# Kernel tuning notes

Hardware: AMD Instinct MI355X
Metric: run time of the kernel (lower is better)

The kernel has to match this reference:

```python
import jax, jax.numpy as jnp
import numpy as np

B = 65536
N_SPARSE = 26
N_DENSE = 13
EMB = 5
VOCAB = 100000
N_EXPERTS = 4
D_IN = N_DENSE + N_SPARSE * EMB  # 143
H1, H2 = 128, 64


def setup_inputs() -> dict:
    key = jax.random.key(0)
    ks = jax.random.split(key, 16)
    s = 0.05
    return {
        "sparse_inputs": jax.random.randint(ks[0], (B, N_SPARSE), 0, VOCAB),
        "dense_inputs": jax.random.normal(ks[1], (B, N_DENSE), dtype=jnp.float32),
        "emb_tables": jax.random.normal(ks[2], (N_SPARSE, VOCAB, EMB), dtype=jnp.float32) * s,
        "expert_W1": jax.random.normal(ks[3], (N_EXPERTS, D_IN, H1), dtype=jnp.float32) * s,
        "expert_b1": jnp.zeros((N_EXPERTS, H1), dtype=jnp.float32),
        "expert_W2": jax.random.normal(ks[4], (N_EXPERTS, H1, H2), dtype=jnp.float32) * s,
        "expert_b2": jnp.zeros((N_EXPERTS, H2), dtype=jnp.float32),
        "gate_finish_W": jax.random.normal(ks[5], (D_IN, N_EXPERTS), dtype=jnp.float32) * s,
        "gate_finish_b": jnp.zeros((N_EXPERTS,), dtype=jnp.float32),
        "gate_like_W": jax.random.normal(ks[6], (D_IN, N_EXPERTS), dtype=jnp.float32) * s,
        "gate_like_b": jnp.zeros((N_EXPERTS,), dtype=jnp.float32),
        "finish_W": jax.random.normal(ks[7], (H2, 1), dtype=jnp.float32) * s,
        "finish_b": jnp.zeros((1,), dtype=jnp.float32),
        "like_W": jax.random.normal(ks[8], (H2, 1), dtype=jnp.float32) * s,
        "like_b": jnp.zeros((1,), dtype=jnp.float32),
    }


def reference(sparse_inputs, dense_inputs, emb_tables, expert_W1, expert_b1,
              expert_W2, expert_b2, gate_finish_W, gate_finish_b,
              gate_like_W, gate_like_b, finish_W, finish_b, like_W, like_b):
    # per-feature embedding lookup: [B, N_SPARSE, EMB]
    feat_idx = jnp.arange(N_SPARSE)[None, :]
    sp_emb = emb_tables[feat_idx, sparse_inputs]
    x = jnp.concatenate([dense_inputs, sp_emb.reshape(sparse_inputs.shape[0], -1)], axis=1)  # [B, D_IN]

    # batched expert MLPs (dropout is inactive at inference)
    h = jax.nn.relu(jnp.einsum('bd,edh->beh', x, expert_W1) + expert_b1)  # [B, E, 128]
    expert_out = jax.nn.relu(jnp.einsum('beh,eho->beo', h, expert_W2) + expert_b2)  # [B, E, 64]

    gate_f = jax.nn.softmax(x @ gate_finish_W + gate_finish_b, axis=-1)  # [B, E]
    gate_l = jax.nn.softmax(x @ gate_like_W + gate_like_b, axis=-1)

    task_finish = jnp.einsum('be,beo->bo', gate_f, expert_out)  # [B, 64]
    task_like = jnp.einsum('be,beo->bo', gate_l, expert_out)

    finish = jax.nn.sigmoid(task_finish @ finish_W + finish_b)  # [B, 1]
    like = jax.nn.sigmoid(task_like @ like_W + like_b)  # [B, 1]
    return finish, like
```

## Files before the change

### kernel.cpp

```cpp
#include <hip/hip_runtime.h>
#include <math.h>

#define NB     65536
#define NSP    26
#define NDN    13
#define EMBD   5
#define VOCAB  100000
#define NE     4
#define DIN    143
#define KPAD   160
#define H1     128
#define H2     64

typedef __attribute__((ext_vector_type(8))) short bf16x8;
typedef __attribute__((ext_vector_type(4))) float f32x4;

__device__ __forceinline__ unsigned short f2bf(float f) {
    unsigned int u = __float_as_uint(f);
    u = (u + 0x7fff + ((u >> 16) & 1)) >> 16;
    return (unsigned short)u;
}

#define E1 (4*8*5*512)
#define E2 (4*4*4*512)
#define E3 (5*512)
#define NWE (E1+E2+E3)
#define GBLKS 1024
#define PBLKS ((NWE+255)/256)


__global__ __launch_bounds__(256)
void gather_pack(const int*   __restrict__ sparse,
                 const float* __restrict__ dense,
                 const float* __restrict__ emb,
                 const float* __restrict__ W1,  const float* __restrict__ W2,
                 const float* __restrict__ gfW, const float* __restrict__ glW,
                 unsigned short* __restrict__ w1p, unsigned short* __restrict__ w2p,
                 unsigned short* __restrict__ gwp, unsigned short* __restrict__ xg)
{
    const int blk = blockIdx.x;
    const int tid = threadIdx.x;
    if (blk < GBLKS) {
        __shared__ int idxs[64 * NSP];
        __shared__ __align__(16) unsigned short xs[64][168];
        const int row0 = blk * 64;

        for (int t = tid; t < 64 * NSP; t += 256)
            idxs[t] = sparse[row0 * NSP + t];
        for (int t = tid; t < 64 * NDN; t += 256) {
            int r = t / NDN, c = t - r * NDN;
            xs[r][c] = f2bf(dense[(row0 + r) * NDN + c]);
        }
        for (int t = tid; t < 64 * (KPAD - DIN); t += 256) {
            int r = t / (KPAD - DIN), c = DIN + (t - r * (KPAD - DIN));
            xs[r][c] = 0;
        }
        __syncthreads();
        for (int t = tid; t < 64 * NSP * EMBD; t += 256) {
            int f = t / (64 * EMBD);
            int rem = t - f * (64 * EMBD);
            int r = rem / EMBD, c = rem - r * EMBD;
            int idx = idxs[r * NSP + f];
            float v = emb[((size_t)f * VOCAB + idx) * EMBD + c];
            xs[r][NDN + f * EMBD + c] = f2bf(v);
        }
        __syncthreads();
        for (int v = tid; v < 4 * 5 * 64; v += 256) {
            int lo = v & 63, chunk = v >> 6;
            int s = chunk % 5, tl = chunk / 5;
            int b = lo & 15, g = lo >> 4;
            bf16x8 val = *(const bf16x8*)&xs[tl * 16 + b][32 * s + 8 * g];
            *(bf16x8*)(xg + ((size_t)((blk * 4 + tl) * 5 + s) * 64 + lo) * 8) = val;
        }
        return;
    }

    int i = (blk - GBLKS) * 256 + tid;
    if (i < E1) {
        int j = i & 7, l = (i >> 3) & 63;
        int rest = i >> 9;
        int s = rest % 5; rest /= 5;
        int nt = rest & 7, e = rest >> 3;
        int b = l & 15, g = l >> 4;
        int k = 32 * s + 8 * g + j;
        int n = nt * 16 + b;
        w1p[i] = (k < DIN) ? f2bf(W1[(e * DIN + k) * H1 + n]) : (unsigned short)0;
        return;
    }
    i -= E1;
    if (i < E2) {
        int j = i & 7, l = (i >> 3) & 63;
        int rest = i >> 9;
        int s = rest & 3; rest >>= 2;
        int ot = rest & 3, e = rest >> 2;
        int b = l & 15, g = l >> 4;
        int k = 32 * s + 8 * g + j;
        int o = ot * 16 + b;
        w2p[i] = f2bf(W2[(e * H1 + k) * H2 + o]);
        return;
    }
    i -= E2;
    if (i < E3) {
        int j = i & 7, l = (i >> 3) & 63;
        int s = i >> 9;
        int b = l & 15, g = l >> 4;
        int k = 32 * s + 8 * g + j;
        float v = 0.f;
        if (k < DIN) {
            if (b < 4)      v = gfW[k * NE + b];
            else if (b < 8) v = glW[k * NE + (b - 4)];
        }
        gwp[i] = f2bf(v);
    }
}

__global__ __launch_bounds__(512, 1)
void mmoe5(const unsigned short* __restrict__ xg,
           const unsigned short* __restrict__ w1p, const float* __restrict__ b1,
           const unsigned short* __restrict__ w2p, const float* __restrict__ b2,
           const unsigned short* __restrict__ gwp,
           const float* __restrict__ gfb, const float* __restrict__ glb,
           const float* __restrict__ fW,  const float* __restrict__ fb,
           const float* __restrict__ lW,  const float* __restrict__ lb,
           float* __restrict__ out)
{
    __shared__ __align__(16) unsigned short wlds[28672];
    __shared__ __align__(16) char hsb[16 * 4096];
    __shared__ float gts[256][8];

    const int tid  = threadIdx.x;
    const int wid  = tid >> 6;
    const int lane = tid & 63;
    const int b    = lane & 15;
    const int g    = lane >> 4;
    const int t0   = blockIdx.x * 16 + wid * 2;
    const int swz  = (b & 7) << 4;
    char* const hw = hsb + (wid * 2) * 4096 + b * 256;

    bf16x8 xf[2][5];
    #pragma unroll
    for (int rt = 0; rt < 2; ++rt)
        #pragma unroll
        for (int s = 0; s < 5; ++s)
            xf[rt][s] = *(const bf16x8*)(xg + ((size_t)((t0 + rt) * 5 + s) * 64 + lane) * 8);

    f32x4 ga[2];
    ga[0] = (f32x4){0.f, 0.f, 0.f, 0.f};
    ga[1] = (f32x4){0.f, 0.f, 0.f, 0.f};
    #pragma unroll
    for (int s = 0; s < 5; ++s) {
        bf16x8 af = *(const bf16x8*)(gwp + (size_t)(s * 64 + lane) * 8);
        ga[0] = __builtin_amdgcn_mfma_f32_16x16x32_bf16(af, xf[0][s], ga[0], 0, 0, 0);
        ga[1] = __builtin_amdgcn_mfma_f32_16x16x32_bf16(af, xf[1][s], ga[1], 0, 0, 0);
    }
    if (g < 2) {
        const float4 bias = *(const float4*)(g ? glb : gfb);
        #pragma unroll
        for (int rt = 0; rt < 2; ++rt) {
            float l0 = ga[rt][0] + bias.x, l1 = ga[rt][1] + bias.y;
            float l2 = ga[rt][2] + bias.z, l3 = ga[rt][3] + bias.w;
            float m = fmaxf(fmaxf(l0, l1), fmaxf(l2, l3));
            float e0 = expf(l0 - m), e1 = expf(l1 - m), e2 = expf(l2 - m), e3 = expf(l3 - m);
            float inv = 1.f / (e0 + e1 + e2 + e3);
            float4 gv; gv.x = e0 * inv; gv.y = e1 * inv; gv.z = e2 * inv; gv.w = e3 * inv;
            *(float4*)&gts[wid * 32 + rt * 16 + b][g * 4] = gv;
        }
    }

    float vf[2] = {0.f, 0.f}, vl[2] = {0.f, 0.f};
    for (int e = 0; e < NE; ++e) {
        __syncthreads();
        #pragma unroll
        for (int v = tid; v < 2560; v += 512)
            *(bf16x8*)(wlds + v * 8) = *(const bf16x8*)(w1p + (size_t)e * 20480 + v * 8);
        #pragma unroll
        for (int v = tid; v < 1024; v += 512)
            *(bf16x8*)(wlds + 20480 + v * 8) = *(const bf16x8*)(w2p + (size_t)e * 8192 + v * 8);
        __syncthreads();

        #pragma unroll
        for (int nt = 0; nt < 8; ++nt) {
            bf16x8 wv[5];
            #pragma unroll
            for (int s = 0; s < 5; ++s)
                wv[s] = *(const bf16x8*)(wlds + ((nt * 5 + s) * 64 + lane) * 8);
            f32x4 acc[2];
            acc[0] = (f32x4){0.f, 0.f, 0.f, 0.f};
            acc[1] = (f32x4){0.f, 0.f, 0.f, 0.f};
            #pragma unroll
            for (int s = 0; s < 5; ++s) {
                acc[0] = __builtin_amdgcn_mfma_f32_16x16x32_bf16(wv[s], xf[0][s], acc[0], 0, 0, 0);
                acc[1] = __builtin_amdgcn_mfma_f32_16x16x32_bf16(wv[s], xf[1][s], acc[1], 0, 0, 0);
            }
            const float4 b1v = *(const float4*)(b1 + e * H1 + nt * 16 + 4 * g);
            #pragma unroll
            for (int rt = 0; rt < 2; ++rt) {
                unsigned lo = (unsigned)f2bf(fmaxf(acc[rt][0] + b1v.x, 0.f)) |
                              ((unsigned)f2bf(fmaxf(acc[rt][1] + b1v.y, 0.f)) << 16);
                unsigned hi = (unsigned)f2bf(fmaxf(acc[rt][2] + b1v.z, 0.f)) |
                              ((unsigned)f2bf(fmaxf(acc[rt][3] + b1v.w, 0.f)) << 16);
                uint2 hv; hv.x = lo; hv.y = hi;
                *(uint2*)(hw + rt * 4096 + ((nt * 32 + g * 8) ^ swz)) = hv;
            }
        }

        bf16x8 hf[2][4];
        #pragma unroll
        for (int rt = 0; rt < 2; ++rt)
            #pragma unroll
            for (int s = 0; s < 4; ++s)
                hf[rt][s] = *(const bf16x8*)(hw + rt * 4096 + ((s * 64 + g * 16) ^ swz));

        float gfv[2], glv[2];
        #pragma unroll
        for (int rt = 0; rt < 2; ++rt) {
            gfv[rt] = gts[wid * 32 + rt * 16 + b][e];
            glv[rt] = gts[wid * 32 + rt * 16 + b][4 + e];
        }

        #pragma unroll
        for (int ot = 0; ot < 4; ++ot) {
            bf16x8 wv2[4];
            #pragma unroll
            for (int s = 0; s < 4; ++s)
                wv2[s] = *(const bf16x8*)(wlds + 20480 + ((ot * 4 + s) * 64 + lane) * 8);
            f32x4 c[2];
            c[0] = (f32x4){0.f, 0.f, 0.f, 0.f};
            c[1] = (f32x4){0.f, 0.f, 0.f, 0.f};
            #pragma unroll
            for (int s = 0; s < 4; ++s) {
                c[0] = __builtin_amdgcn_mfma_f32_16x16x32_bf16(wv2[s], hf[0][s], c[0], 0, 0, 0);
                c[1] = __builtin_amdgcn_mfma_f32_16x16x32_bf16(wv2[s], hf[1][s], c[1], 0, 0, 0);
            }
            const float4 b2v = *(const float4*)(b2 + e * H2 + ot * 16 + 4 * g);
            const float4 fwv = *(const float4*)(fW + ot * 16 + 4 * g);
            const float4 lwv = *(const float4*)(lW + ot * 16 + 4 * g);
            #pragma unroll
            for (int rt = 0; rt < 2; ++rt) {
                float o0 = fmaxf(c[rt][0] + b2v.x, 0.f), o1 = fmaxf(c[rt][1] + b2v.y, 0.f);
                float o2 = fmaxf(c[rt][2] + b2v.z, 0.f), o3 = fmaxf(c[rt][3] + b2v.w, 0.f);
                vf[rt] += gfv[rt] * (o0 * fwv.x + o1 * fwv.y + o2 * fwv.z + o3 * fwv.w);
                vl[rt] += glv[rt] * (o0 * lwv.x + o1 * lwv.y + o2 * lwv.z + o3 * lwv.w);
            }
        }
    }

    #pragma unroll
    for (int rt = 0; rt < 2; ++rt) {
        float f = vf[rt], l = vl[rt];
        f += __shfl_xor(f, 16); f += __shfl_xor(f, 32);
        l += __shfl_xor(l, 16); l += __shfl_xor(l, 32);
        if (g == 0) {
            int r = (t0 + rt) * 16 + b;
            out[r]      = 1.f / (1.f + expf(-(f + fb[0])));
            out[NB + r] = 1.f / (1.f + expf(-(l + lb[0])));
        }
    }
}


__global__ __launch_bounds__(256)
void preproc(const float* __restrict__ W1, const float* __restrict__ W2,
             const float* __restrict__ gfW, const float* __restrict__ glW,
             unsigned short* __restrict__ w1t, unsigned short* __restrict__ w2t,
             unsigned short* __restrict__ gwc)
{
    int i = blockIdx.x * 256 + threadIdx.x;
    if (i < 4*128*160) {
        int k = i % KPAD;
        int n = (i / KPAD) & (H1 - 1);
        int e = i / (KPAD * H1);
        w1t[i] = (k < DIN) ? f2bf(W1[(e * DIN + k) * H1 + n]) : (unsigned short)0;
    } else if (i < 4*128*160 + 4*64*128) {
        int j = i - 4*128*160;
        int k = j & (H1 - 1);
        int o = (j >> 7) & (H2 - 1);
        int e = j >> 13;
        w2t[j] = f2bf(W2[(e * H1 + k) * H2 + o]);
    } else if (i < 4*128*160 + 4*64*128 + 16*160) {
        int j = i - (4*128*160 + 4*64*128);
        int k = j % KPAD;
        int r = j / KPAD;
        float v = 0.f;
        if (k < DIN) {
            if (r < 4)      v = gfW[k * NE + r];
            else if (r < 8) v = glW[k * NE + (r - 4)];
        }
        gwc[j] = f2bf(v);
    }
}

__global__ __launch_bounds__(256)
void mmoe_mfma(const int*   __restrict__ sparse,
               const float* __restrict__ dense,
               const float* __restrict__ emb,
               const unsigned short* __restrict__ w1t,
               const float* __restrict__ b1,
               const unsigned short* __restrict__ w2t,
               const float* __restrict__ b2,
               const unsigned short* __restrict__ gwc,
               const float* __restrict__ gfb, const float* __restrict__ glb,
               const float* __restrict__ fW,  const float* __restrict__ fb,
               const float* __restrict__ lW,  const float* __restrict__ lb,
               float* __restrict__ out)
{
    __shared__ __align__(16) unsigned short xs[64][KPAD];
    __shared__ __align__(16) unsigned short hs[64][136];
    __shared__ __align__(16) float gts[64][8];

    const int tid   = threadIdx.x;
    const int wid   = tid >> 6;
    const int lane  = tid & 63;
    const int b     = lane & 15;
    const int g     = lane >> 4;
    const int rbase = wid * 16;
    const int grow0 = blockIdx.x * 64 + rbase;

    for (int t = lane; t < 16 * NDN; t += 64) {
        int r = t & 15, d = t >> 4;
        xs[rbase + r][d] = f2bf(dense[(grow0 + r) * NDN + d]);
    }
    for (int t = lane; t < 16 * (KPAD - DIN); t += 64) {
        int r = t & 15, d = DIN + (t >> 4);
        xs[rbase + r][d] = 0;
    }
    for (int t = lane; t < 16 * NSP; t += 64) {
        int r = t & 15, f = t >> 4;
        int idx = sparse[(grow0 + r) * NSP + f];
        const float* ep = emb + (f * VOCAB + idx) * EMBD;
        int c0 = NDN + EMBD * f;
        #pragma unroll
        for (int c = 0; c < EMBD; ++c)
            xs[rbase + r][c0 + c] = f2bf(ep[c]);
    }

    bf16x8 xf[5];
    #pragma unroll
    for (int s = 0; s < 5; ++s)
        xf[s] = *(const bf16x8*)&xs[rbase + b][32 * s + 8 * g];

    f32x4 ga = {0.f, 0.f, 0.f, 0.f};
    #pragma unroll
    for (int s = 0; s < 5; ++s) {
        bf16x8 af = *(const bf16x8*)(gwc + b * KPAD + 32 * s + 8 * g);
        ga = __builtin_amdgcn_mfma_f32_16x16x32_bf16(af, xf[s], ga, 0, 0, 0);
    }
    if (g < 2) {
        const float4 bias = *(const float4*)(g ? glb : gfb);
        float l0 = ga[0] + bias.x, l1 = ga[1] + bias.y;
        float l2 = ga[2] + bias.z, l3 = ga[3] + bias.w;
        float m = fmaxf(fmaxf(l0, l1), fmaxf(l2, l3));
        float e0 = expf(l0 - m), e1 = expf(l1 - m), e2 = expf(l2 - m), e3 = expf(l3 - m);
        float inv = 1.f / (e0 + e1 + e2 + e3);
        float4 gv; gv.x = e0 * inv; gv.y = e1 * inv; gv.z = e2 * inv; gv.w = e3 * inv;
        *(float4*)&gts[rbase + b][g * 4] = gv;
    }

    float vf = 0.f, vl = 0.f;
    for (int e = 0; e < NE; ++e) {
        const unsigned short* w1e = w1t + e * (H1 * KPAD);
        #pragma unroll
        for (int nt = 0; nt < 8; ++nt) {
            f32x4 acc = {0.f, 0.f, 0.f, 0.f};
            #pragma unroll
            for (int s = 0; s < 5; ++s) {
                bf16x8 af = *(const bf16x8*)(w1e + (nt * 16 + b) * KPAD + 32 * s + 8 * g);
                acc = __builtin_amdgcn_mfma_f32_16x16x32_bf16(af, xf[s], acc, 0, 0, 0);
            }
            const float4 b1v = *(const float4*)(b1 + e * H1 + nt * 16 + 4 * g);
            unsigned lo = (unsigned)f2bf(fmaxf(acc[0] + b1v.x, 0.f)) |
                          ((unsigned)f2bf(fmaxf(acc[1] + b1v.y, 0.f)) << 16);
            unsigned hi = (unsigned)f2bf(fmaxf(acc[2] + b1v.z, 0.f)) |
                          ((unsigned)f2bf(fmaxf(acc[3] + b1v.w, 0.f)) << 16);
            uint2 hv; hv.x = lo; hv.y = hi;
            *(uint2*)&hs[rbase + b][nt * 16 + 4 * g] = hv;
        }

        bf16x8 hf[4];
        #pragma unroll
        for (int s = 0; s < 4; ++s)
            hf[s] = *(const bf16x8*)&hs[rbase + b][32 * s + 8 * g];

        float gf = gts[rbase + b][e];
        float gl = gts[rbase + b][4 + e];
        const unsigned short* w2e = w2t + e * (H2 * H1);
        #pragma unroll
        for (int ot = 0; ot < 4; ++ot) {
            f32x4 acc = {0.f, 0.f, 0.f, 0.f};
            #pragma unroll
            for (int s = 0; s < 4; ++s) {
                bf16x8 af = *(const bf16x8*)(w2e + (ot * 16 + b) * H1 + 32 * s + 8 * g);
                acc = __builtin_amdgcn_mfma_f32_16x16x32_bf16(af, hf[s], acc, 0, 0, 0);
            }
            const float4 b2v = *(const float4*)(b2 + e * H2 + ot * 16 + 4 * g);
            const float4 fwv = *(const float4*)(fW + ot * 16 + 4 * g);
            const float4 lwv = *(const float4*)(lW + ot * 16 + 4 * g);
            float o0 = fmaxf(acc[0] + b2v.x, 0.f);
            float o1 = fmaxf(acc[1] + b2v.y, 0.f);
            float o2 = fmaxf(acc[2] + b2v.z, 0.f);
            float o3 = fmaxf(acc[3] + b2v.w, 0.f);
            vf += gf * (o0 * fwv.x + o1 * fwv.y + o2 * fwv.z + o3 * fwv.w);
            vl += gl * (o0 * lwv.x + o1 * lwv.y + o2 * lwv.z + o3 * lwv.w);
        }
    }

    vf += __shfl_xor(vf, 16); vf += __shfl_xor(vf, 32);
    vl += __shfl_xor(vl, 16); vl += __shfl_xor(vl, 32);
    if (g == 0) {
        int r = grow0 + b;
        out[r]      = 1.f / (1.f + expf(-(vf + fb[0])));
        out[NB + r] = 1.f / (1.f + expf(-(vl + lb[0])));
    }
}


extern "C" void kernel_launch(void* const* d_in, const int* in_sizes, int n_in,
                              void* d_out, int out_size, void* d_ws, size_t ws_size,
                              hipStream_t stream) {
    const int*   sparse = (const int*)  d_in[0];
    const float* dense  = (const float*)d_in[1];
    const float* emb    = (const float*)d_in[2];
    const float* W1     = (const float*)d_in[3];
    const float* b1     = (const float*)d_in[4];
    const float* W2     = (const float*)d_in[5];
    const float* b2     = (const float*)d_in[6];
    const float* gfW    = (const float*)d_in[7];
    const float* gfb    = (const float*)d_in[8];
    const float* glW    = (const float*)d_in[9];
    const float* glb    = (const float*)d_in[10];
    const float* fW     = (const float*)d_in[11];
    const float* fb     = (const float*)d_in[12];
    const float* lW     = (const float*)d_in[13];
    const float* lb     = (const float*)d_in[14];

    const size_t XG_BYTES = (size_t)NB * KPAD * 2;
    const size_t NEED = XG_BYTES + (size_t)NWE * 2;

    if (ws_size >= NEED) {
        unsigned short* xg  = (unsigned short*)d_ws;
        unsigned short* w1p = (unsigned short*)((char*)d_ws + XG_BYTES);
        unsigned short* w2p = (unsigned short*)((char*)d_ws + XG_BYTES + (size_t)E1 * 2);
        unsigned short* gwp = (unsigned short*)((char*)d_ws + XG_BYTES + (size_t)(E1 + E2) * 2);

        gather_pack<<<GBLKS + PBLKS, 256, 0, stream>>>(
            sparse, dense, emb, W1, W2, gfW, glW, w1p, w2p, gwp, xg);
        mmoe5<<<NB / 256, 512, 0, stream>>>(xg, w1p, b1, w2p, b2, gwp,
                                            gfb, glb, fW, fb, lW, lb,
                                            (float*)d_out);
    } else {
        unsigned short* w1t = (unsigned short*)d_ws;
        unsigned short* w2t = (unsigned short*)((char*)d_ws + 163840);
        unsigned short* gwc = (unsigned short*)((char*)d_ws + 229376);

        int tot = 4*128*160 + 4*64*128 + 16*160;
        preproc<<<(tot + 255) / 256, 256, 0, stream>>>(W1, W2, gfW, glW, w1t, w2t, gwc);
        mmoe_mfma<<<NB / 64, 256, 0, stream>>>(sparse, dense, emb,
                                               w1t, b1, w2t, b2, gwc,
                                               gfb, glb, fW, fb, lW, lb,
                                               (float*)d_out);
    }
}
```

Before: 62.97 us.

## Prefetch next expert weights into registers, split layer-2 into halves, smaller blocks

The MMoE kernel now runs 256-thread blocks with two blocks per CU (was one 512-thread block), each covering 128 rows. The next expert's weights are prefetched into registers while the current expert computes, so global loads overlap with the MFMA work. The hidden layer is split into two halves with layer-2 accumulation done per half, which halves the LDS staging buffer for activations. Bf16 packing now uses the hardware v_cvt_pk_bf16_f32 instruction instead of software rounding. In exchange, register pressure rises from the prefetch buffers and layer-2 accumulators, and each weight tile is loaded by twice as many blocks.

```diff
diff --git a/kernel.cpp b/kernel.cpp
--- a/kernel.cpp
+++ b/kernel.cpp
@@ -19,6 +19,12 @@
     unsigned int u = __float_as_uint(f);
     u = (u + 0x7fff + ((u >> 16) & 1)) >> 16;
     return (unsigned short)u;
+}
+
+__device__ __forceinline__ unsigned cvtpk(float lo, float hi) {
+    unsigned r;
+    asm("v_cvt_pk_bf16_f32 %0, %1, %2" : "=v"(r) : "v"(lo), "v"(hi));
+    return r;
 }
 
 #define E1 (4*8*5*512)
@@ -114,8 +120,8 @@
     }
 }
 
-__global__ __launch_bounds__(512, 1)
-void mmoe5(const unsigned short* __restrict__ xg,
+__global__ __launch_bounds__(256, 2)
+void mmoe7(const unsigned short* __restrict__ xg,
            const unsigned short* __restrict__ w1p, const float* __restrict__ b1,
            const unsigned short* __restrict__ w2p, const float* __restrict__ b2,
            const unsigned short* __restrict__ gwp,
@@ -124,18 +130,18 @@
            const float* __restrict__ lW,  const float* __restrict__ lb,
            float* __restrict__ out)
 {
-    __shared__ __align__(16) unsigned short wlds[28672];
-    __shared__ __align__(16) char hsb[16 * 4096];
-    __shared__ float gts[256][8];
+    __shared__ __align__(16) char wlds[57344];
+    __shared__ __align__(16) char hsb[16384];
+    __shared__ float gts[128][8];
 
     const int tid  = threadIdx.x;
     const int wid  = tid >> 6;
     const int lane = tid & 63;
     const int b    = lane & 15;
     const int g    = lane >> 4;
-    const int t0   = blockIdx.x * 16 + wid * 2;
+    const int t0   = blockIdx.x * 8 + wid * 2;
     const int swz  = (b & 7) << 4;
-    char* const hw = hsb + (wid * 2) * 4096 + b * 256;
+    char* const hw = hsb + wid * 4096 + b * 128;
 
     bf16x8 xf[2][5];
     #pragma unroll
@@ -143,6 +149,14 @@
         #pragma unroll
         for (int s = 0; s < 5; ++s)
             xf[rt][s] = *(const bf16x8*)(xg + ((size_t)((t0 + rt) * 5 + s) * 64 + lane) * 8);
+
+    bf16x8 pw1[10], pw2[4];
+    #pragma unroll
+    for (int i = 0; i < 10; ++i)
+        pw1[i] = *(const bf16x8*)(w1p + (size_t)(tid + i * 256) * 8);
+    #pragma unroll
+    for (int i = 0; i < 4; ++i)
+        pw2[i] = *(const bf16x8*)(w2p + (size_t)(tid + i * 256) * 8);
 
     f32x4 ga[2];
     ga[0] = (f32x4){0.f, 0.f, 0.f, 0.f};
@@ -171,45 +185,70 @@
     for (int e = 0; e < NE; ++e) {
         __syncthreads();
         #pragma unroll
-        for (int v = tid; v < 2560; v += 512)
-            *(bf16x8*)(wlds + v * 8) = *(const bf16x8*)(w1p + (size_t)e * 20480 + v * 8);
-        #pragma unroll
-        for (int v = tid; v < 1024; v += 512)
-            *(bf16x8*)(wlds + 20480 + v * 8) = *(const bf16x8*)(w2p + (size_t)e * 8192 + v * 8);
+        for (int i = 0; i < 10; ++i)
+            *(bf16x8*)(wlds + (tid + i * 256) * 16) = pw1[i];
+        #pragma unroll
+        for (int i = 0; i < 4; ++i)
+            *(bf16x8*)(wlds + 40960 + (tid + i * 256) * 16) = pw2[i];
+        if (e < 3) {
+            #pragma unroll
+            for (int i = 0; i < 10; ++i)
+                pw1[i] = *(const bf16x8*)(w1p + (size_t)(e + 1) * 20480 + (size_t)(tid + i * 256) * 8);
+            #pragma unroll
+            for (int i = 0; i < 4; ++i)
+                pw2[i] = *(const bf16x8*)(w2p + (size_t)(e + 1) * 8192 + (size_t)(tid + i * 256) * 8);
+        }
         __syncthreads();
 
-        #pragma unroll
-        for (int nt = 0; nt < 8; ++nt) {
-            bf16x8 wv[5];
-            #pragma unroll
-            for (int s = 0; s < 5; ++s)
-                wv[s] = *(const bf16x8*)(wlds + ((nt * 5 + s) * 64 + lane) * 8);
-            f32x4 acc[2];
-            acc[0] = (f32x4){0.f, 0.f, 0.f, 0.f};
-            acc[1] = (f32x4){0.f, 0.f, 0.f, 0.f};
-            #pragma unroll
-            for (int s = 0; s < 5; ++s) {
-                acc[0] = __builtin_amdgcn_mfma_f32_16x16x32_bf16(wv[s], xf[0][s], acc[0], 0, 0, 0);
-                acc[1] = __builtin_amdgcn_mfma_f32_16x16x32_bf16(wv[s], xf[1][s], acc[1], 0, 0, 0);
+        f32x4 c[2][4];
+        #pragma unroll
+        for (int rt = 0; rt < 2; ++rt)
+            #pragma unroll
+            for (int ot = 0; ot < 4; ++ot)
+                c[rt][ot] = (f32x4){0.f, 0.f, 0.f, 0.f};
+
+        #pragma unroll
+        for (int h = 0; h < 2; ++h) {
+            #pragma unroll
+            for (int nl = 0; nl < 4; ++nl) {
+                const int nt = h * 4 + nl;
+                bf16x8 wv[5];
+                #pragma unroll
+                for (int s = 0; s < 5; ++s)
+                    wv[s] = *(const bf16x8*)(wlds + ((nt * 5 + s) * 64 + lane) * 16);
+                f32x4 acc[2];
+                acc[0] = (f32x4){0.f, 0.f, 0.f, 0.f};
+                acc[1] = (f32x4){0.f, 0.f, 0.f, 0.f};
+                #pragma unroll
+                for (int s = 0; s < 5; ++s) {
+                    acc[0] = __builtin_amdgcn_mfma_f32_16x16x32_bf16(wv[s], xf[0][s], acc[0], 0, 0, 0);
+                    acc[1] = __builtin_amdgcn_mfma_f32_16x16x32_bf16(wv[s], xf[1][s], acc[1], 0, 0, 0);
+                }
+                const float4 b1v = *(const float4*)(b1 + e * H1 + nt * 16 + 4 * g);
+                #pragma unroll
+                for (int rt = 0; rt < 2; ++rt) {
+                    uint2 hv;
+                    hv.x = cvtpk(fmaxf(acc[rt][0] + b1v.x, 0.f), fmaxf(acc[rt][1] + b1v.y, 0.f));
+                    hv.y = cvtpk(fmaxf(acc[rt][2] + b1v.z, 0.f), fmaxf(acc[rt][3] + b1v.w, 0.f));
+                    *(uint2*)(hw + rt * 2048 + ((nl * 32 + g * 8) ^ swz)) = hv;
+                }
             }
-            const float4 b1v = *(const float4*)(b1 + e * H1 + nt * 16 + 4 * g);
-            #pragma unroll
-            for (int rt = 0; rt < 2; ++rt) {
-                unsigned lo = (unsigned)f2bf(fmaxf(acc[rt][0] + b1v.x, 0.f)) |
-                              ((unsigned)f2bf(fmaxf(acc[rt][1] + b1v.y, 0.f)) << 16);
-                unsigned hi = (unsigned)f2bf(fmaxf(acc[rt][2] + b1v.z, 0.f)) |
-                              ((unsigned)f2bf(fmaxf(acc[rt][3] + b1v.w, 0.f)) << 16);
-                uint2 hv; hv.x = lo; hv.y = hi;
-                *(uint2*)(hw + rt * 4096 + ((nt * 32 + g * 8) ^ swz)) = hv;
+            bf16x8 hf[2][2];
+            #pragma unroll
+            for (int sl = 0; sl < 2; ++sl)
+                #pragma unroll
+                for (int rt = 0; rt < 2; ++rt)
+                    hf[sl][rt] = *(const bf16x8*)(hw + rt * 2048 + ((sl * 64 + g * 16) ^ swz));
+            #pragma unroll
+            for (int ot = 0; ot < 4; ++ot) {
+                #pragma unroll
+                for (int sl = 0; sl < 2; ++sl) {
+                    bf16x8 wv2 = *(const bf16x8*)(wlds + 40960 + ((ot * 4 + h * 2 + sl) * 64 + lane) * 16);
+                    c[0][ot] = __builtin_amdgcn_mfma_f32_16x16x32_bf16(wv2, hf[sl][0], c[0][ot], 0, 0, 0);
+                    c[1][ot] = __builtin_amdgcn_mfma_f32_16x16x32_bf16(wv2, hf[sl][1], c[1][ot], 0, 0, 0);
+                }
             }
         }
-
-        bf16x8 hf[2][4];
-        #pragma unroll
-        for (int rt = 0; rt < 2; ++rt)
-            #pragma unroll
-            for (int s = 0; s < 4; ++s)
-                hf[rt][s] = *(const bf16x8*)(hw + rt * 4096 + ((s * 64 + g * 16) ^ swz));
 
         float gfv[2], glv[2];
         #pragma unroll
@@ -217,28 +256,15 @@
             gfv[rt] = gts[wid * 32 + rt * 16 + b][e];
             glv[rt] = gts[wid * 32 + rt * 16 + b][4 + e];
         }
-
         #pragma unroll
         for (int ot = 0; ot < 4; ++ot) {
-            bf16x8 wv2[4];
-            #pragma unroll
-            for (int s = 0; s < 4; ++s)
-                wv2[s] = *(const bf16x8*)(wlds + 20480 + ((ot * 4 + s) * 64 + lane) * 8);
-            f32x4 c[2];
-            c[0] = (f32x4){0.f, 0.f, 0.f, 0.f};
-            c[1] = (f32x4){0.f, 0.f, 0.f, 0.f};
-            #pragma unroll
-            for (int s = 0; s < 4; ++s) {
-                c[0] = __builtin_amdgcn_mfma_f32_16x16x32_bf16(wv2[s], hf[0][s], c[0], 0, 0, 0);
-                c[1] = __builtin_amdgcn_mfma_f32_16x16x32_bf16(wv2[s], hf[1][s], c[1], 0, 0, 0);
-            }
             const float4 b2v = *(const float4*)(b2 + e * H2 + ot * 16 + 4 * g);
             const float4 fwv = *(const float4*)(fW + ot * 16 + 4 * g);
             const float4 lwv = *(const float4*)(lW + ot * 16 + 4 * g);
             #pragma unroll
             for (int rt = 0; rt < 2; ++rt) {
-                float o0 = fmaxf(c[rt][0] + b2v.x, 0.f), o1 = fmaxf(c[rt][1] + b2v.y, 0.f);
-                float o2 = fmaxf(c[rt][2] + b2v.z, 0.f), o3 = fmaxf(c[rt][3] + b2v.w, 0.f);
+                float o0 = fmaxf(c[rt][ot][0] + b2v.x, 0.f), o1 = fmaxf(c[rt][ot][1] + b2v.y, 0.f);
+                float o2 = fmaxf(c[rt][ot][2] + b2v.z, 0.f), o3 = fmaxf(c[rt][ot][3] + b2v.w, 0.f);
                 vf[rt] += gfv[rt] * (o0 * fwv.x + o1 * fwv.y + o2 * fwv.z + o3 * fwv.w);
                 vl[rt] += glv[rt] * (o0 * lwv.x + o1 * lwv.y + o2 * lwv.z + o3 * lwv.w);
             }
@@ -444,7 +470,7 @@
 
         gather_pack<<<GBLKS + PBLKS, 256, 0, stream>>>(
             sparse, dense, emb, W1, W2, gfW, glW, w1p, w2p, gwp, xg);
-        mmoe5<<<NB / 256, 512, 0, stream>>>(xg, w1p, b1, w2p, b2, gwp,
+        mmoe7<<<NB / 128, 256, 0, stream>>>(xg, w1p, b1, w2p, b2, gwp,
                                             gfb, glb, fW, fb, lW, lb,
                                             (float*)d_out);
     } else {
```

After: 58.58 us. 7.0% less time.
